# Kernel tuning notes

Hardware: AMD Instinct MI355X
Metric: run time of the kernel (lower is better)

Reference implementation:

```python
import jax, jax.numpy as jnp
import numpy as np

B, S, C, L = 8, 256, 4, 256
E, H, NL, NS = 256, 8, 2, 8
DH = E // H
EPS = 1e-5


def _conv1d(x, w, b):
    # x: [B, Cin, L], w: [Cout, Cin, K] -> [B, Cout, L] (SAME padding, stride 1)
    y = jax.lax.conv_general_dilated(x, w, (1,), 'SAME', dimension_numbers=('NCH', 'OIH', 'NCH'))
    return y + b[None, :, None]


def _local_cnn(xs, w1, b1, w2, b2):
    # xs: [B, 4, L] for one segment; per-segment weights
    h = jax.nn.relu(_conv1d(xs, w1, b1))
    h = jax.nn.relu(_conv1d(h, w2, b2))
    return jnp.max(h, axis=-1)  # AdaptiveMaxPool1d(1) + squeeze -> [B, E]


def _layernorm(x, g, b):
    m = jnp.mean(x, axis=-1, keepdims=True)
    v = jnp.mean((x - m) ** 2, axis=-1, keepdims=True)
    return (x - m) / jnp.sqrt(v + EPS) * g + b


def setup_inputs() -> dict:
    key = jax.random.key(0)
    ks = jax.random.split(key, 24)
    n = lambda k, shp, s: jax.random.normal(k, shp, jnp.float32) * s
    return {
        'x': jax.random.normal(ks[0], (B, S, C, L), jnp.float32),
        'conv1_w': n(ks[1], (S, 128, 4, 3), 0.1), 'conv1_b': jnp.zeros((S, 128), jnp.float32),
        'conv2_w': n(ks[2], (S, E, 128, 3), 0.05), 'conv2_b': jnp.zeros((S, E), jnp.float32),
        'ln1_g': jnp.ones((NL, E), jnp.float32), 'ln1_b': jnp.zeros((NL, E), jnp.float32),
        'wq': n(ks[3], (NL, E, E), 0.02), 'bq': jnp.zeros((NL, E), jnp.float32),
        'wk': n(ks[4], (NL, E, E), 0.02), 'bk': jnp.zeros((NL, E), jnp.float32),
        'wv': n(ks[5], (NL, E, E), 0.02), 'bv': jnp.zeros((NL, E), jnp.float32),
        'wo': n(ks[6], (NL, E, E), 0.02), 'bo': jnp.zeros((NL, E), jnp.float32),
        'bias_w': n(ks[7], (NL, 4, H), 0.1), 'bias_b': jnp.zeros((NL, H), jnp.float32),
        'ln2_g': jnp.ones((NL, E), jnp.float32), 'ln2_b': jnp.zeros((NL, E), jnp.float32),
        'ffn_w1': n(ks[8], (NL, E, 2 * E), 0.02), 'ffn_b1': jnp.zeros((NL, 2 * E), jnp.float32),
        'ffn_w2': n(ks[9], (NL, 2 * E, E), 0.02), 'ffn_b2': jnp.zeros((NL, E), jnp.float32),
        'fc_w': n(ks[10], (NS * E, 2), 0.02), 'fc_b': jnp.zeros((2,), jnp.float32),
    }


def _forward(x, conv1_w, conv1_b, conv2_w, conv2_b, ln1_g, ln1_b,
             wq, bq, wk, bk, wv, bv, wo, bo, bias_w, bias_b,
             ln2_g, ln2_b, ffn_w1, ffn_b1, ffn_w2, ffn_b2, fc_w, fc_b):
    # Per-segment CNNs (vmap over segment axis with per-segment weights) -> [B, S, E]
    cnn = jax.vmap(_local_cnn, in_axes=(1, 0, 0, 0, 0), out_axes=1)(x, conv1_w, conv1_b, conv2_w, conv2_b)
    feat = _layernorm(cnn, jnp.ones((E,), cnn.dtype), jnp.zeros((E,), cnn.dtype))  # F.layer_norm, no affine

    # bias matrices: cdist (p=2), global-max normalized; positional distance; inverses
    sq = jnp.sum(feat * feat, axis=-1)  # [B, S]
    d2 = sq[:, :, None] + sq[:, None, :] - 2.0 * jnp.einsum('bie,bje->bij', feat, feat)
    dist = jnp.sqrt(jnp.maximum(d2, 0.0))
    dist = dist / (jnp.max(dist) + 1e-6)
    idx = jnp.arange(S, dtype=feat.dtype)
    rdist = jnp.abs(idx[:, None] - idx[None, :]) / (S - 1)
    rdist = jnp.broadcast_to(rdist[None], (feat.shape[0], S, S))
    attn_bias = jnp.stack([dist, rdist, 1.0 - rdist, 1.0 - dist], axis=-1)  # [B,S,S,4]

    h = feat
    scale = 1.0 / jnp.sqrt(jnp.asarray(DH, h.dtype))
    for l in range(NL):
        hn = _layernorm(h, ln1_g[l], ln1_b[l])
        q = (hn @ wq[l] + bq[l]).reshape(-1, S, H, DH)
        k = (hn @ wk[l] + bk[l]).reshape(-1, S, H, DH)
        v = (hn @ wv[l] + bv[l]).reshape(-1, S, H, DH)
        scores = jnp.einsum('bihd,bjhd->bhij', q, k) * scale
        scores = scores + jnp.einsum('bijc,ch->bhij', attn_bias, bias_w[l]) + bias_b[l][None, :, None, None]
        a = jax.nn.softmax(scores, axis=-1)
        o = jnp.einsum('bhij,bjhd->bihd', a, v).reshape(-1, S, E) @ wo[l] + bo[l]
        h = h + o
        hn2 = _layernorm(h, ln2_g[l], ln2_b[l])
        f = jax.nn.relu(hn2 @ ffn_w1[l] + ffn_b1[l]) @ ffn_w2[l] + ffn_b2[l]
        h = h + f

    # split into NS chunks along segments, max-pool each, concat (S % NS == 0)
    pooled = jnp.max(h.reshape(-1, NS, S // NS, E), axis=2).reshape(-1, NS * E)
    return pooled @ fc_w + fc_b  # [B, num_classes]


def reference(x, conv1_w, conv1_b, conv2_w, conv2_b, ln1_g, ln1_b,
              wq, bq, wk, bk, wv, bv, wo, bo, bias_w, bias_b,
              ln2_g, ln2_b, ffn_w1, ffn_b1, ffn_w2, ffn_b2, fc_w, fc_b):
    return _forward(x, conv1_w, conv1_b, conv2_w, conv2_b, ln1_g, ln1_b,
                    wq, bq, wk, bk, wv, bv, wo, bo, bias_w, bias_b,
                    ln2_g, ln2_b, ffn_w1, ffn_b1, ffn_w2, ffn_b2, fc_w, fc_b)
```

## Files before the change

kernel.cpp:

```cpp
#include <hip/hip_runtime.h>
#include <hip/hip_bf16.h>


typedef float floatx4 __attribute__((ext_vector_type(4)));
typedef short bf16x8 __attribute__((ext_vector_type(8)));

__device__ __forceinline__ float wave_sum(float v) {
    v += __shfl_xor(v, 32); v += __shfl_xor(v, 16); v += __shfl_xor(v, 8);
    v += __shfl_xor(v, 4);  v += __shfl_xor(v, 2);  v += __shfl_xor(v, 1);
    return v;
}
__device__ __forceinline__ float wave_max(float v) {
    v = fmaxf(v, __shfl_xor(v, 32)); v = fmaxf(v, __shfl_xor(v, 16));
    v = fmaxf(v, __shfl_xor(v, 8));  v = fmaxf(v, __shfl_xor(v, 4));
    v = fmaxf(v, __shfl_xor(v, 2));  v = fmaxf(v, __shfl_xor(v, 1));
    return v;
}
__device__ __forceinline__ unsigned short f2bf(float v) {
    unsigned b = __float_as_uint(v);
    unsigned r = (b + 0x7fffu + ((b >> 16) & 1u)) >> 16;
    return (unsigned short)r;
}

typedef const __attribute__((address_space(1))) unsigned int* gas_u32p;
typedef __attribute__((address_space(3))) unsigned int* las_u32p;

__device__ __forceinline__ void stage_chunk(const unsigned short* gbase,
                                            unsigned short* lbase,
                                            int wv, int lane)
{
    const char* g = (const char*)gbase + (wv << 11) + (lane << 4);
    char* l = (char*)lbase + (wv << 11);
    __builtin_amdgcn_global_load_lds((gas_u32p)(const void*)g,
                                     (las_u32p)(void*)l, 16, 0, 0);
    __builtin_amdgcn_global_load_lds((gas_u32p)(const void*)(g + 1024),
                                     (las_u32p)(void*)(l + 1024), 16, 0, 0);
}

__global__ void init_kernel(unsigned* dmax, unsigned* cnnmax) {
    const size_t i = (size_t)blockIdx.x * 256 + threadIdx.x;
    cnnmax[i] = 0u;
    if (i == 0) *dmax = 0u;
}

__global__ __launch_bounds__(256) void prep_w2_kernel(
    const float* __restrict__ w2, unsigned short* __restrict__ w2b)
{
    const int s = blockIdx.x;
    const int part = blockIdx.y;
    const float* src = w2 + (size_t)s * 98304;
    unsigned short* dst = w2b + (size_t)s * 98304;
    for (int o = part * 24576 + threadIdx.x; o < (part + 1) * 24576; o += 256) {
        const int c  = o >> 13;
        const int w  = o & 8191;
        const int co = w >> 5;
        const int up = (w >> 3) & 3;
        const int t  = w & 7;
        const int u  = (up ^ co ^ (co >> 2)) & 3;
        const int kk = c * 32 + u * 8 + t;
        const int ci = kk & 127, tap = kk >> 7;
        dst[o] = f2bf(src[(size_t)co * 384 + ci * 3 + tap]);
    }
}

__global__ __launch_bounds__(512, 4) void conv2_fused_kernel(
    const unsigned short* __restrict__ w2b,
    const float* __restrict__ x,
    const float* __restrict__ w1,
    const float* __restrict__ b1,
    const float* __restrict__ b2,
    unsigned* __restrict__ cnnmax)
{
    __shared__ float xs[4][258];
    __shared__ float w1s[1536];
    __shared__ unsigned short Hs[130 * 136];
    __shared__ unsigned short Ab[2][8192];

    const int tid = threadIdx.x;
    const int lane = tid & 63;
    const int wv = __builtin_amdgcn_readfirstlane((int)(tid >> 6));
    const int wm = wv & 3, wn = wv >> 2;
    const int bid = blockIdx.x;
    const int xcd = bid & 7;
    const int pos = bid >> 3;
    const int s   = xcd * 32 + (pos >> 4);
    const int nt  = pos & 15;
    const int b = nt >> 1;
    const int l0 = (nt & 1) * 128;
    const int lr = lane & 15;
    const int quad = lane >> 4;
    const int qk = quad * 8;

    const float* xp = x + ((size_t)(b * 256 + s)) * 1024;
    for (int i = tid; i < 1024; i += 512) {
        const int ci = i >> 8, l = i & 255;
        xs[ci][l + 1] = xp[i];
    }
    if (tid < 4) { xs[tid][0] = 0.f; xs[tid][257] = 0.f; }
    const float* w1p = w1 + (size_t)s * 1536;
    for (int i = tid; i < 1536; i += 512) w1s[i] = w1p[i];
    const int co1 = tid & 127;
    const float bb1 = b1[s * 128 + co1];
    __syncthreads();

    const unsigned short* wchunks = w2b + (size_t)s * 98304;
    stage_chunk(wchunks, &Ab[0][0], wv, lane);

    {
        const int g = tid >> 7;
        float wreg[12];
#pragma unroll
        for (int k = 0; k < 12; k++) wreg[k] = w1s[co1 * 12 + k];
        for (int pr = g; pr < 130; pr += 4) {
            const int l = l0 - 1 + pr;
            float a = 0.f;
            if ((unsigned)l < 256u) {
                a = bb1;
#pragma unroll
                for (int ci = 0; ci < 4; ci++)
#pragma unroll
                    for (int k = 0; k < 3; k++) a = fmaf(wreg[ci * 3 + k], xs[ci][l + k], a);
                a = fmaxf(a, 0.f);
            }
            Hs[pr * 136 + co1] = f2bf(a);
        }
    }

    floatx4 acc[4][4];
#pragma unroll
    for (int r = 0; r < 4; r++)
#pragma unroll
        for (int c = 0; c < 4; c++) acc[r][c] = (floatx4){0.f, 0.f, 0.f, 0.f};

    const int nb = wn * 64;
    const int aoff = wm * 2048 + lr * 32 + (((quad ^ lr ^ (lr >> 2)) & 3) * 8);
    const int hbase = (nb + lr) * 136 + qk;

    asm volatile("s_waitcnt vmcnt(0) lgkmcnt(0)" ::: "memory");
    __builtin_amdgcn_s_barrier();
    __builtin_amdgcn_sched_barrier(0);

#pragma unroll
    for (int ks = 0; ks < 12; ks++) {
        if (ks) {
            asm volatile("s_waitcnt vmcnt(0)" ::: "memory");
            __builtin_amdgcn_s_barrier();
            __builtin_amdgcn_sched_barrier(0);
        }
        if (ks < 11)
            stage_chunk(wchunks + (size_t)(ks + 1) * 8192, &Ab[(ks + 1) & 1][0], wv, lane);
        const int tap_ = ks >> 2, ci0_ = (ks & 3) * 32;
        const unsigned short* ap = &Ab[ks & 1][aoff];
        const unsigned short* hp = &Hs[hbase + tap_ * 136 + ci0_];
        bf16x8 a[4], bb[4];
#pragma unroll
        for (int r = 0; r < 4; r++) a[r] = *(const bf16x8*)(ap + r * 512);
#pragma unroll
        for (int c = 0; c < 4; c++) bb[c] = *(const bf16x8*)(hp + c * 2176);
#pragma unroll
        for (int r = 0; r < 4; r++)
#pragma unroll
            for (int c = 0; c < 4; c++)
                acc[r][c] = __builtin_amdgcn_mfma_f32_16x16x32_bf16(
                    a[r], bb[c], acc[r][c], 0, 0, 0);
    }

    const float* b2s = b2 + s * 256;
    unsigned* cmrow = cnnmax + ((size_t)(b * 256 + s)) * 256;
#pragma unroll
    for (int r = 0; r < 4; r++) {
#pragma unroll
        for (int e = 0; e < 4; e++) {
            const int co = wm * 64 + r * 16 + quad * 4 + e;
            const float bias = b2s[co];
            float mv = 0.f;
#pragma unroll
            for (int c = 0; c < 4; c++) mv = fmaxf(mv, acc[r][c][e] + bias);
            mv = fmaxf(mv, __shfl_xor(mv, 1));
            mv = fmaxf(mv, __shfl_xor(mv, 2));
            mv = fmaxf(mv, __shfl_xor(mv, 4));
            mv = fmaxf(mv, __shfl_xor(mv, 8));
            if (lr == 0) atomicMax(&cmrow[co], __float_as_uint(mv));
        }
    }
}

__global__ __launch_bounds__(256) void ln0_kernel(
    const unsigned* __restrict__ cm, float* __restrict__ out, float* __restrict__ sqv)
{
    const int tid = threadIdx.x, lane = tid & 63, wid = tid >> 6;
    const int row = blockIdx.x * 4 + wid;
    const unsigned* xr = cm + (size_t)row * 256;
    float v[4];
#pragma unroll
    for (int i = 0; i < 4; i++) v[i] = __uint_as_float(xr[lane + 64 * i]);
    float sm = wave_sum(v[0] + v[1] + v[2] + v[3]);
    const float mean = sm * (1.f / 256.f);
    float qv = 0.f;
#pragma unroll
    for (int i = 0; i < 4; i++) { const float d = v[i] - mean; qv = fmaf(d, d, qv); }
    qv = wave_sum(qv);
    const float inv = rsqrtf(qv * (1.f / 256.f) + 1e-5f);
    float* orow = out + (size_t)row * 256;
#pragma unroll
    for (int i = 0; i < 4; i++) orow[lane + 64 * i] = (v[i] - mean) * inv;
    if (lane == 0) sqv[row] = qv * inv * inv;
}

__global__ __launch_bounds__(256) void dist_kernel(
    const float* __restrict__ feat, const float* __restrict__ sq,
    float* __restrict__ dist, unsigned* __restrict__ dmax)
{
    __shared__ float Fi[32][260];
    __shared__ float Fj[16][260];
    __shared__ float redm[4];
    const int tid = threadIdx.x;
    const int bid = blockIdx.x;
    const int b = bid >> 7, it = (bid >> 4) & 7, jt = bid & 15;
    const float* fb = feat + (size_t)b * 65536;
    for (int idx = tid; idx < 32 * 256; idx += 256) {
        const int r = idx >> 8, e = idx & 255;
        Fi[r][e] = fb[(it * 32 + r) * 256 + e];
    }
    for (int idx = tid; idx < 16 * 256; idx += 256) {
        const int r = idx >> 8, e = idx & 255;
        Fj[r][e] = fb[(jt * 16 + r) * 256 + e];
    }
    __syncthreads();
    const int ii = tid >> 3, j0 = (tid & 7) * 2;
    float acc[2] = {0.f, 0.f};
    for (int e = 0; e < 256; e += 4) {
        const float4 a = *(const float4*)&Fi[ii][e];
#pragma unroll
        for (int u = 0; u < 2; u++) {
            const float4 bv = *(const float4*)&Fj[j0 + u][e];
            acc[u] += a.x * bv.x + a.y * bv.y + a.z * bv.z + a.w * bv.w;
        }
    }
    const float sqi = sq[b * 256 + it * 32 + ii];
    float mymax = 0.f;
#pragma unroll
    for (int u = 0; u < 2; u++) {
        const float d2 = sqi + sq[b * 256 + jt * 16 + j0 + u] - 2.f * acc[u];
        const float d = sqrtf(fmaxf(d2, 0.f));
        dist[((size_t)b * 256 + it * 32 + ii) * 256 + jt * 16 + j0 + u] = d;
        mymax = fmaxf(mymax, d);
    }
    mymax = wave_max(mymax);
    if ((tid & 63) == 0) redm[tid >> 6] = mymax;
    __syncthreads();
    if (tid == 0) {
        const float m = fmaxf(fmaxf(redm[0], redm[1]), fmaxf(redm[2], redm[3]));
        atomicMax(dmax, __float_as_uint(m));
    }
}

__global__ __launch_bounds__(256) void ln_bf_kernel(
    const float* __restrict__ x, const float* __restrict__ g, const float* __restrict__ bta,
    unsigned short* __restrict__ out)
{
    const int tid = threadIdx.x, lane = tid & 63, wid = tid >> 6;
    const int row = blockIdx.x * 4 + wid;
    const float* xr = x + (size_t)row * 256;
    float v[4];
#pragma unroll
    for (int i = 0; i < 4; i++) v[i] = xr[lane + 64 * i];
    float sm = wave_sum(v[0] + v[1] + v[2] + v[3]);
    const float mean = sm * (1.f / 256.f);
    float q = 0.f;
#pragma unroll
    for (int i = 0; i < 4; i++) { const float d = v[i] - mean; q = fmaf(d, d, q); }
    q = wave_sum(q);
    const float inv = rsqrtf(q * (1.f / 256.f) + 1e-5f);
    unsigned short* orow = out + (size_t)row * 256;
#pragma unroll
    for (int i = 0; i < 4; i++) {
        const int e = lane + 64 * i;
        orow[e] = f2bf((v[i] - mean) * inv * g[e] + bta[e]);
    }
}

__global__ __launch_bounds__(256) void prep_wt_kernel(
    const float* __restrict__ wq, const float* __restrict__ wk, const float* __restrict__ wv,
    const float* __restrict__ wo, const float* __restrict__ f1, const float* __restrict__ f2,
    unsigned short* __restrict__ wtb)
{
    __shared__ float t[32][33];
    const int z = blockIdx.z;
    const int l = z / 6, id = z % 6;
    const float* src; int K_, N_; size_t doff;
    switch (id) {
        case 0:  src = wq + (size_t)l * 65536;  K_ = 256; N_ = 256; doff = 0;      break;
        case 1:  src = wk + (size_t)l * 65536;  K_ = 256; N_ = 256; doff = 65536;  break;
        case 2:  src = wv + (size_t)l * 65536;  K_ = 256; N_ = 256; doff = 131072; break;
        case 3:  src = wo + (size_t)l * 65536;  K_ = 256; N_ = 256; doff = 196608; break;
        case 4:  src = f1 + (size_t)l * 131072; K_ = 256; N_ = 512; doff = 262144; break;
        default: src = f2 + (size_t)l * 131072; K_ = 512; N_ = 256; doff = 393216; break;
    }
    const int k0 = blockIdx.x * 32, n0 = blockIdx.y * 32;
    if (k0 >= K_ || n0 >= N_) return;
    unsigned short* dst = wtb + (size_t)l * 524288 + doff;
    const int c = threadIdx.x & 31, rq = threadIdx.x >> 5;
#pragma unroll
    for (int i = 0; i < 4; i++) {
        const int r = rq + i * 8;
        t[r][c] = src[(size_t)(k0 + r) * N_ + n0 + c];
    }
    __syncthreads();
#pragma unroll
    for (int i = 0; i < 4; i++) {
        const int r = rq + i * 8;
        dst[(size_t)(n0 + r) * K_ + k0 + c] = f2bf(t[c][r]);
    }
}

__global__ __launch_bounds__(128) void gemm_mfma_kernel(
    const unsigned short* __restrict__ A, const unsigned short* __restrict__ Wt,
    const float* __restrict__ b0, const float* __restrict__ b1, const float* __restrict__ b2,
    const float* __restrict__ R, float* __restrict__ outf,
    unsigned short* __restrict__ o0, unsigned short* __restrict__ o1, unsigned short* __restrict__ o2,
    int K, int mode)
{
    const int tid = threadIdx.x;
    const int lane = tid & 63, lr = lane & 15, quad = lane >> 4;
    const int wv = __builtin_amdgcn_readfirstlane((int)(tid >> 6));
    const int m0 = blockIdx.x * 128 + wv * 64;
    const int n0 = blockIdx.y * 32;

    floatx4 acc[4][2];
#pragma unroll
    for (int r = 0; r < 4; r++)
#pragma unroll
        for (int c = 0; c < 2; c++) acc[r][c] = (floatx4){0.f, 0.f, 0.f, 0.f};

    const unsigned short* Ap = A + (size_t)(m0 + lr) * K + quad * 8;
    const unsigned short* Bp = Wt + (size_t)(n0 + lr) * K + quad * 8;
    const int nks = K >> 5;
#pragma unroll 4
    for (int ks = 0; ks < nks; ks++) {
        const int ko = ks * 32;
        bf16x8 a[4], b[2];
#pragma unroll
        for (int r = 0; r < 4; r++) a[r] = *(const bf16x8*)(Ap + (size_t)r * 16 * K + ko);
#pragma unroll
        for (int c = 0; c < 2; c++) b[c] = *(const bf16x8*)(Bp + (size_t)c * 16 * K + ko);
#pragma unroll
        for (int r = 0; r < 4; r++)
#pragma unroll
            for (int c = 0; c < 2; c++)
                acc[r][c] = __builtin_amdgcn_mfma_f32_16x16x32_bf16(a[r], b[c], acc[r][c], 0, 0, 0);
    }

    if (mode == 0) {
        const int which = n0 >> 8, nn0 = n0 & 255;
        if (which < 2) {
            unsigned short* op = which ? o1 : o0;
            const float* bp = which ? b1 : b0;
#pragma unroll
            for (int r = 0; r < 4; r++)
#pragma unroll
                for (int c = 0; c < 2; c++)
#pragma unroll
                    for (int e = 0; e < 4; e++) {
                        const int m = m0 + r * 16 + quad * 4 + e;
                        const int n = nn0 + c * 16 + lr;
                        op[(size_t)m * 256 + n] = f2bf(acc[r][c][e] + bp[n]);
                    }
        } else {
#pragma unroll
            for (int r = 0; r < 4; r++)
#pragma unroll
                for (int c = 0; c < 2; c++)
#pragma unroll
                    for (int e = 0; e < 4; e++) {
                        const int m = m0 + r * 16 + quad * 4 + e;
                        const int nn = nn0 + c * 16 + lr;
                        const int bb_ = m >> 8, j = m & 255, hh = nn >> 5, d = nn & 31;
                        o2[(size_t)((bb_ * 8 + hh) * 32 + d) * 256 + j] = f2bf(acc[r][c][e] + b2[nn]);
                    }
        }
    } else if (mode == 1) {
#pragma unroll
        for (int r = 0; r < 4; r++)
#pragma unroll
            for (int c = 0; c < 2; c++)
#pragma unroll
                for (int e = 0; e < 4; e++) {
                    const int m = m0 + r * 16 + quad * 4 + e;
                    const int n = n0 + c * 16 + lr;
                    outf[(size_t)m * 256 + n] = acc[r][c][e] + b0[n] + R[(size_t)m * 256 + n];
                }
    } else {
#pragma unroll
        for (int r = 0; r < 4; r++)
#pragma unroll
            for (int c = 0; c < 2; c++)
#pragma unroll
                for (int e = 0; e < 4; e++) {
                    const int m = m0 + r * 16 + quad * 4 + e;
                    const int n = n0 + c * 16 + lr;
                    o0[(size_t)m * 512 + n] = f2bf(fmaxf(acc[r][c][e] + b0[n], 0.f));
                }
    }
}

__global__ __launch_bounds__(256) void attn_mfma_kernel(
    const unsigned short* __restrict__ q_bf, const unsigned short* __restrict__ k_bf,
    const unsigned short* __restrict__ vt_bf,
    const float* __restrict__ dist, const unsigned* __restrict__ dmax,
    const float* __restrict__ bw, const float* __restrict__ bb,
    unsigned short* __restrict__ ao_bf)
{
    __shared__ unsigned short Ps[4][16][264];
    const int tid = threadIdx.x;
    const int lane = tid & 63, lr = lane & 15, quad = lane >> 4;
    const int wv = __builtin_amdgcn_readfirstlane((int)(tid >> 6));
    const int ic = blockIdx.x, hh = blockIdx.y, b = blockIdx.z;
    const int i0 = ic * 64 + wv * 16;

    const float dinv = 1.f / (__uint_as_float(*dmax) + 1e-6f);
    const float w0 = bw[0 * 8 + hh], w1 = bw[1 * 8 + hh], w2 = bw[2 * 8 + hh], w3 = bw[3 * 8 + hh];
    const float bbh = bb[hh];
    const float scale = 0.17677669529663687f;

    const bf16x8 aq = *(const bf16x8*)(q_bf + (size_t)(b * 256 + i0 + lr) * 256 + hh * 32 + quad * 8);
    floatx4 sc[16];
#pragma unroll
    for (int c = 0; c < 16; c++) {
        const bf16x8 bk = *(const bf16x8*)(k_bf + (size_t)(b * 256 + c * 16 + lr) * 256 + hh * 32 + quad * 8);
        sc[c] = __builtin_amdgcn_mfma_f32_16x16x32_bf16(aq, bk, (floatx4){0.f, 0.f, 0.f, 0.f}, 0, 0, 0);
    }

#pragma unroll
    for (int e = 0; e < 4; e++) {
        const int i = i0 + quad * 4 + e;
        const float* drow = dist + ((size_t)(b * 256 + i)) * 256;
        float bs[16];
        float mx = -1e30f;
#pragma unroll
        for (int c = 0; c < 16; c++) {
            const int j = c * 16 + lr;
            const float dn = drow[j] * dinv;
            const float rd = fabsf((float)(i - j)) * (1.f / 255.f);
            bs[c] = sc[c][e] * scale + w0 * dn + w1 * rd + w2 * (1.f - rd) + w3 * (1.f - dn) + bbh;
            mx = fmaxf(mx, bs[c]);
        }
        mx = fmaxf(mx, __shfl_xor(mx, 1)); mx = fmaxf(mx, __shfl_xor(mx, 2));
        mx = fmaxf(mx, __shfl_xor(mx, 4)); mx = fmaxf(mx, __shfl_xor(mx, 8));
        float sm = 0.f;
#pragma unroll
        for (int c = 0; c < 16; c++) { bs[c] = __expf(bs[c] - mx); sm += bs[c]; }
        sm += __shfl_xor(sm, 1); sm += __shfl_xor(sm, 2);
        sm += __shfl_xor(sm, 4); sm += __shfl_xor(sm, 8);
        const float rs = 1.f / sm;
#pragma unroll
        for (int c = 0; c < 16; c++)
            Ps[wv][quad * 4 + e][c * 16 + lr] = f2bf(bs[c] * rs);
    }
    __syncthreads();

    floatx4 oc[2];
    oc[0] = (floatx4){0.f, 0.f, 0.f, 0.f};
    oc[1] = (floatx4){0.f, 0.f, 0.f, 0.f};
    const unsigned short* vtb = vt_bf + (size_t)(b * 8 + hh) * 8192;
#pragma unroll
    for (int ks = 0; ks < 8; ks++) {
        const bf16x8 ap = *(const bf16x8*)(&Ps[wv][lr][ks * 32 + quad * 8]);
#pragma unroll
        for (int c2 = 0; c2 < 2; c2++) {
            const bf16x8 bvv = *(const bf16x8*)(vtb + (size_t)(c2 * 16 + lr) * 256 + ks * 32 + quad * 8);
            oc[c2] = __builtin_amdgcn_mfma_f32_16x16x32_bf16(ap, bvv, oc[c2], 0, 0, 0);
        }
    }
#pragma unroll
    for (int c2 = 0; c2 < 2; c2++)
#pragma unroll
        for (int e = 0; e < 4; e++)
            ao_bf[(size_t)(b * 256 + i0 + quad * 4 + e) * 256 + hh * 32 + c2 * 16 + lr] = f2bf(oc[c2][e]);
}

__global__ __launch_bounds__(256) void pool_fc_kernel(
    const float* __restrict__ h, const float* __restrict__ fcw,
    const float* __restrict__ fcb, float* __restrict__ out)
{
    __shared__ float red[8];
    const int b = blockIdx.x, tid = threadIdx.x, lane = tid & 63, wid = tid >> 6;
    float a0 = 0.f, a1 = 0.f;
    for (int ns = 0; ns < 8; ns++) {
        const float* hp = h + ((size_t)(b * 256 + ns * 32)) * 256 + tid;
        float m = hp[0];
#pragma unroll
        for (int r = 1; r < 32; r++) m = fmaxf(m, hp[(size_t)r * 256]);
        a0 = fmaf(m, fcw[(ns * 256 + tid) * 2 + 0], a0);
        a1 = fmaf(m, fcw[(ns * 256 + tid) * 2 + 1], a1);
    }
    a0 = wave_sum(a0);
    a1 = wave_sum(a1);
    if (lane == 0) { red[wid] = a0; red[4 + wid] = a1; }
    __syncthreads();
    if (tid == 0) out[b * 2 + 0] = red[0] + red[1] + red[2] + red[3] + fcb[0];
    if (tid == 1) out[b * 2 + 1] = red[4] + red[5] + red[6] + red[7] + fcb[1];
}

extern "C" void kernel_launch(void* const* d_in, const int* in_sizes, int n_in,
                              void* d_out, int out_size, void* d_ws, size_t ws_size,
                              hipStream_t stream)
{
    (void)in_sizes; (void)n_in; (void)out_size; (void)ws_size;
    const float* x       = (const float*)d_in[0];
    const float* conv1_w = (const float*)d_in[1];
    const float* conv1_b = (const float*)d_in[2];
    const float* conv2_w = (const float*)d_in[3];
    const float* conv2_b = (const float*)d_in[4];
    const float* ln1_g   = (const float*)d_in[5];
    const float* ln1_b   = (const float*)d_in[6];
    const float* wq = (const float*)d_in[7];  const float* bq = (const float*)d_in[8];
    const float* wk = (const float*)d_in[9];  const float* bk = (const float*)d_in[10];
    const float* wvp = (const float*)d_in[11]; const float* bv = (const float*)d_in[12];
    const float* wo = (const float*)d_in[13]; const float* bo = (const float*)d_in[14];
    const float* bias_w = (const float*)d_in[15];
    const float* bias_b = (const float*)d_in[16];
    const float* ln2_g  = (const float*)d_in[17];
    const float* ln2_b  = (const float*)d_in[18];
    const float* ffn_w1 = (const float*)d_in[19]; const float* ffn_b1 = (const float*)d_in[20];
    const float* ffn_w2 = (const float*)d_in[21]; const float* ffn_b2 = (const float*)d_in[22];
    const float* fc_w   = (const float*)d_in[23]; const float* fc_b = (const float*)d_in[24];
    float* out = (float*)d_out;

    float* ws = (float*)d_ws;
    float* h    = ws;
    float* dist = h + 524288;
    float* sqv  = dist + 524288;
    unsigned* dmax = (unsigned*)(sqv + 2048);
    unsigned* cnnmax = (unsigned*)(sqv + 2048 + 16);
    unsigned short* hn_bf = (unsigned short*)(sqv + 2048 + 16 + 524288);
    unsigned short* q_bf  = hn_bf + 524288;
    unsigned short* k_bf  = q_bf + 524288;
    unsigned short* vt_bf = k_bf + 524288;
    unsigned short* ao_bf = vt_bf + 524288;
    unsigned short* fm_bf = ao_bf + 524288;
    unsigned short* wtb   = fm_bf + 1048576;
    unsigned short* w2b   = wtb + 1048576;

    init_kernel<<<2048, 256, 0, stream>>>(dmax, cnnmax);
    prep_wt_kernel<<<dim3(16, 16, 12), 256, 0, stream>>>(wq, wk, wvp, wo, ffn_w1, ffn_w2, wtb);
    prep_w2_kernel<<<dim3(256, 4), 256, 0, stream>>>(conv2_w, w2b);
    conv2_fused_kernel<<<4096, 512, 0, stream>>>(
        w2b, x, conv1_w, conv1_b, conv2_b, cnnmax);
    ln0_kernel<<<512, 256, 0, stream>>>(cnnmax, h, sqv);
    dist_kernel<<<1024, 256, 0, stream>>>(h, sqv, dist, dmax);

    for (int l = 0; l < 2; l++) {
        const unsigned short* wqkvT = wtb + (size_t)l * 524288;
        const unsigned short* woT   = wqkvT + 196608;
        const unsigned short* f1T   = wqkvT + 262144;
        const unsigned short* f2T   = wqkvT + 393216;

        ln_bf_kernel<<<512, 256, 0, stream>>>(h, ln1_g + l * 256, ln1_b + l * 256, hn_bf);
        gemm_mfma_kernel<<<dim3(16, 24), 128, 0, stream>>>(
            hn_bf, wqkvT, bq + l * 256, bk + l * 256, bv + l * 256,
            nullptr, nullptr, q_bf, k_bf, vt_bf, 256, 0);
        attn_mfma_kernel<<<dim3(4, 8, 8), 256, 0, stream>>>(
            q_bf, k_bf, vt_bf, dist, dmax, bias_w + l * 32, bias_b + l * 8, ao_bf);
        gemm_mfma_kernel<<<dim3(16, 8), 128, 0, stream>>>(
            ao_bf, woT, bo + l * 256, nullptr, nullptr,
            h, h, nullptr, nullptr, nullptr, 256, 1);
        ln_bf_kernel<<<512, 256, 0, stream>>>(h, ln2_g + l * 256, ln2_b + l * 256, hn_bf);
        gemm_mfma_kernel<<<dim3(16, 16), 128, 0, stream>>>(
            hn_bf, f1T, ffn_b1 + l * 512, nullptr, nullptr,
            nullptr, nullptr, fm_bf, nullptr, nullptr, 256, 2);
        gemm_mfma_kernel<<<dim3(16, 8), 128, 0, stream>>>(
            fm_bf, f2T, ffn_b2 + l * 256, nullptr, nullptr,
            h, h, nullptr, nullptr, nullptr, 512, 1);
    }
    pool_fc_kernel<<<8, 256, 0, stream>>>(h, fc_w, fc_b, out);
}
```

Measured before the change: 568.2 us.

## Merge prep kernels, add MFMA setprio, shrink GEMM tiles for more blocks

Folds the init, weight-transpose and conv2-weight prep kernels into one launch that dispatches on block index, removing two launches. Wraps the conv2 MFMA loop in s_setprio so waves issuing matrix ops get scheduling priority. Halves the GEMM M tile per wave (64 to 32 rows) and doubles the grid, so the small transformer GEMMs spread across more CUs at the cost of reloading the B operand more often.

```diff
diff --git a/kernel.cpp b/kernel.cpp
--- a/kernel.cpp
+++ b/kernel.cpp
@@ -37,29 +37,73 @@
                                      (las_u32p)(void*)(l + 1024), 16, 0, 0);
 }
 
-__global__ void init_kernel(unsigned* dmax, unsigned* cnnmax) {
-    const size_t i = (size_t)blockIdx.x * 256 + threadIdx.x;
-    cnnmax[i] = 0u;
-    if (i == 0) *dmax = 0u;
-}
-
-__global__ __launch_bounds__(256) void prep_w2_kernel(
+__global__ __launch_bounds__(256) void prep_all_kernel(
+    unsigned* __restrict__ dmax, unsigned* __restrict__ cnnmax,
+    const float* __restrict__ wq, const float* __restrict__ wk,
+    const float* __restrict__ wv, const float* __restrict__ wo,
+    const float* __restrict__ f1, const float* __restrict__ f2,
+    unsigned short* __restrict__ wtb,
     const float* __restrict__ w2, unsigned short* __restrict__ w2b)
 {
-    const int s = blockIdx.x;
-    const int part = blockIdx.y;
-    const float* src = w2 + (size_t)s * 98304;
-    unsigned short* dst = w2b + (size_t)s * 98304;
-    for (int o = part * 24576 + threadIdx.x; o < (part + 1) * 24576; o += 256) {
-        const int c  = o >> 13;
-        const int w  = o & 8191;
-        const int co = w >> 5;
-        const int up = (w >> 3) & 3;
-        const int t  = w & 7;
-        const int u  = (up ^ co ^ (co >> 2)) & 3;
-        const int kk = c * 32 + u * 8 + t;
-        const int ci = kk & 127, tap = kk >> 7;
-        dst[o] = f2bf(src[(size_t)co * 384 + ci * 3 + tap]);
+    __shared__ float t[32][33];
+    const int bid = blockIdx.x;
+    const int tid = threadIdx.x;
+
+    if (bid < 2048) {
+        const size_t i = (size_t)bid * 256 + tid;
+        cnnmax[i] = 0u;
+        if (i == 0) *dmax = 0u;
+        return;
+    }
+    if (bid < 5120) {
+        const int idx = bid - 2048;
+        const int z = idx >> 8;
+        const int by = (idx >> 4) & 15;
+        const int bx = idx & 15;
+        const int l = z / 6, id = z % 6;
+        const float* src; int K_, N_; size_t doff;
+        switch (id) {
+            case 0:  src = wq + (size_t)l * 65536;  K_ = 256; N_ = 256; doff = 0;      break;
+            case 1:  src = wk + (size_t)l * 65536;  K_ = 256; N_ = 256; doff = 65536;  break;
+            case 2:  src = wv + (size_t)l * 65536;  K_ = 256; N_ = 256; doff = 131072; break;
+            case 3:  src = wo + (size_t)l * 65536;  K_ = 256; N_ = 256; doff = 196608; break;
+            case 4:  src = f1 + (size_t)l * 131072; K_ = 256; N_ = 512; doff = 262144; break;
+            default: src = f2 + (size_t)l * 131072; K_ = 512; N_ = 256; doff = 393216; break;
+        }
+        const int k0 = bx * 32, n0 = by * 32;
+        if (k0 >= K_ || n0 >= N_) return;
+        unsigned short* dst = wtb + (size_t)l * 524288 + doff;
+        const int c = tid & 31, rq = tid >> 5;
+#pragma unroll
+        for (int i = 0; i < 4; i++) {
+            const int r = rq + i * 8;
+            t[r][c] = src[(size_t)(k0 + r) * N_ + n0 + c];
+        }
+        __syncthreads();
+#pragma unroll
+        for (int i = 0; i < 4; i++) {
+            const int r = rq + i * 8;
+            dst[(size_t)(n0 + r) * K_ + k0 + c] = f2bf(t[c][r]);
+        }
+        return;
+    }
+    {
+        const int idx = bid - 5120;
+        const int s = idx & 255;
+        const int part = idx >> 8;
+        const float* src = w2 + (size_t)s * 98304;
+        unsigned short* dst = w2b + (size_t)s * 98304;
+        for (int o = part * 24576 + tid; o < (part + 1) * 24576; o += 256) {
+            const int c  = o >> 13;
+            const int w  = o & 8191;
+            const int co = w >> 5;
+            const int up = (w >> 3) & 3;
+            const int tt = w & 7;
+            const int u  = (up ^ co ^ (co >> 2)) & 3;
+            const int kk = c * 32 + u * 8 + tt;
+            const int ci = kk & 127, tap = kk >> 7;
+            dst[o] = f2bf(src[(size_t)co * 384 + ci * 3 + tap]);
+        }
     }
 }
 
@@ -157,12 +201,14 @@
         for (int r = 0; r < 4; r++) a[r] = *(const bf16x8*)(ap + r * 512);
 #pragma unroll
         for (int c = 0; c < 4; c++) bb[c] = *(const bf16x8*)(hp + c * 2176);
+        __builtin_amdgcn_s_setprio(1);
 #pragma unroll
         for (int r = 0; r < 4; r++)
 #pragma unroll
             for (int c = 0; c < 4; c++)
                 acc[r][c] = __builtin_amdgcn_mfma_f32_16x16x32_bf16(
                     a[r], bb[c], acc[r][c], 0, 0, 0);
+        __builtin_amdgcn_s_setprio(0);
     }
 
     const float* b2s = b2 + s * 256;
@@ -280,40 +326,6 @@
     }
 }
 
-__global__ __launch_bounds__(256) void prep_wt_kernel(
-    const float* __restrict__ wq, const float* __restrict__ wk, const float* __restrict__ wv,
-    const float* __restrict__ wo, const float* __restrict__ f1, const float* __restrict__ f2,
-    unsigned short* __restrict__ wtb)
-{
-    __shared__ float t[32][33];
-    const int z = blockIdx.z;
-    const int l = z / 6, id = z % 6;
-    const float* src; int K_, N_; size_t doff;
-    switch (id) {
-        case 0:  src = wq + (size_t)l * 65536;  K_ = 256; N_ = 256; doff = 0;      break;
-        case 1:  src = wk + (size_t)l * 65536;  K_ = 256; N_ = 256; doff = 65536;  break;
-        case 2:  src = wv + (size_t)l * 65536;  K_ = 256; N_ = 256; doff = 131072; break;
-        case 3:  src = wo + (size_t)l * 65536;  K_ = 256; N_ = 256; doff = 196608; break;
-        case 4:  src = f1 + (size_t)l * 131072; K_ = 256; N_ = 512; doff = 262144; break;
-        default: src = f2 + (size_t)l * 131072; K_ = 512; N_ = 256; doff = 393216; break;
-    }
-    const int k0 = blockIdx.x * 32, n0 = blockIdx.y * 32;
-    if (k0 >= K_ || n0 >= N_) return;
-    unsigned short* dst = wtb + (size_t)l * 524288 + doff;
-    const int c = threadIdx.x & 31, rq = threadIdx.x >> 5;
-#pragma unroll
-    for (int i = 0; i < 4; i++) {
-        const int r = rq + i * 8;
-        t[r][c] = src[(size_t)(k0 + r) * N_ + n0 + c];
-    }
-    __syncthreads();
-#pragma unroll
-    for (int i = 0; i < 4; i++) {
-        const int r = rq + i * 8;
-        dst[(size_t)(n0 + r) * K_ + k0 + c] = f2bf(t[c][r]);
-    }
-}
-
 __global__ __launch_bounds__(128) void gemm_mfma_kernel(
     const unsigned short* __restrict__ A, const unsigned short* __restrict__ Wt,
     const float* __restrict__ b0, const float* __restrict__ b1, const float* __restrict__ b2,
@@ -324,12 +336,12 @@
     const int tid = threadIdx.x;
     const int lane = tid & 63, lr = lane & 15, quad = lane >> 4;
     const int wv = __builtin_amdgcn_readfirstlane((int)(tid >> 6));
-    const int m0 = blockIdx.x * 128 + wv * 64;
+    const int m0 = blockIdx.x * 64 + wv * 32;
     const int n0 = blockIdx.y * 32;
 
-    floatx4 acc[4][2];
-#pragma unroll
-    for (int r = 0; r < 4; r++)
+    floatx4 acc[2][2];
+#pragma unroll
+    for (int r = 0; r < 2; r++)
 #pragma unroll
         for (int c = 0; c < 2; c++) acc[r][c] = (floatx4){0.f, 0.f, 0.f, 0.f};
 
@@ -339,13 +351,13 @@
 #pragma unroll 4
     for (int ks = 0; ks < nks; ks++) {
         const int ko = ks * 32;
-        bf16x8 a[4], b[2];
-#pragma unroll
-        for (int r = 0; r < 4; r++) a[r] = *(const bf16x8*)(Ap + (size_t)r * 16 * K + ko);
+        bf16x8 a[2], b[2];
+#pragma unroll
+        for (int r = 0; r < 2; r++) a[r] = *(const bf16x8*)(Ap + (size_t)r * 16 * K + ko);
 #pragma unroll
         for (int c = 0; c < 2; c++) b[c] = *(const bf16x8*)(Bp + (size_t)c * 16 * K + ko);
 #pragma unroll
-        for (int r = 0; r < 4; r++)
+        for (int r = 0; r < 2; r++)
 #pragma unroll
             for (int c = 0; c < 2; c++)
                 acc[r][c] = __builtin_amdgcn_mfma_f32_16x16x32_bf16(a[r], b[c], acc[r][c], 0, 0, 0);
@@ -357,7 +369,7 @@
             unsigned short* op = which ? o1 : o0;
             const float* bp = which ? b1 : b0;
 #pragma unroll
-            for (int r = 0; r < 4; r++)
+            for (int r = 0; r < 2; r++)
 #pragma unroll
                 for (int c = 0; c < 2; c++)
 #pragma unroll
@@ -368,7 +380,7 @@
                     }
         } else {
 #pragma unroll
-            for (int r = 0; r < 4; r++)
+            for (int r = 0; r < 2; r++)
 #pragma unroll
                 for (int c = 0; c < 2; c++)
 #pragma unroll
@@ -381,7 +393,7 @@
         }
     } else if (mode == 1) {
 #pragma unroll
-        for (int r = 0; r < 4; r++)
+        for (int r = 0; r < 2; r++)
 #pragma unroll
             for (int c = 0; c < 2; c++)
 #pragma unroll
@@ -392,7 +404,7 @@
                 }
     } else {
 #pragma unroll
-        for (int r = 0; r < 4; r++)
+        for (int r = 0; r < 2; r++)
 #pragma unroll
             for (int c = 0; c < 2; c++)
 #pragma unroll
@@ -542,9 +554,8 @@
     unsigned short* wtb   = fm_bf + 1048576;
     unsigned short* w2b   = wtb + 1048576;
 
-    init_kernel<<<2048, 256, 0, stream>>>(dmax, cnnmax);
-    prep_wt_kernel<<<dim3(16, 16, 12), 256, 0, stream>>>(wq, wk, wvp, wo, ffn_w1, ffn_w2, wtb);
-    prep_w2_kernel<<<dim3(256, 4), 256, 0, stream>>>(conv2_w, w2b);
+    prep_all_kernel<<<6144, 256, 0, stream>>>(
+        dmax, cnnmax, wq, wk, wvp, wo, ffn_w1, ffn_w2, wtb, conv2_w, w2b);
     conv2_fused_kernel<<<4096, 512, 0, stream>>>(
         w2b, x, conv1_w, conv1_b, conv2_b, cnnmax);
     ln0_kernel<<<512, 256, 0, stream>>>(cnnmax, h, sqv);
@@ -557,19 +568,19 @@
         const unsigned short* f2T   = wqkvT + 393216;
 
         ln_bf_kernel<<<512, 256, 0, stream>>>(h, ln1_g + l * 256, ln1_b + l * 256, hn_bf);
-        gemm_mfma_kernel<<<dim3(16, 24), 128, 0, stream>>>(
+        gemm_mfma_kernel<<<dim3(32, 24), 128, 0, stream>>>(
             hn_bf, wqkvT, bq + l * 256, bk + l * 256, bv + l * 256,
             nullptr, nullptr, q_bf, k_bf, vt_bf, 256, 0);
         attn_mfma_kernel<<<dim3(4, 8, 8), 256, 0, stream>>>(
             q_bf, k_bf, vt_bf, dist, dmax, bias_w + l * 32, bias_b + l * 8, ao_bf);
-        gemm_mfma_kernel<<<dim3(16, 8), 128, 0, stream>>>(
+        gemm_mfma_kernel<<<dim3(32, 8), 128, 0, stream>>>(
             ao_bf, woT, bo + l * 256, nullptr, nullptr,
             h, h, nullptr, nullptr, nullptr, 256, 1);
         ln_bf_kernel<<<512, 256, 0, stream>>>(h, ln2_g + l * 256, ln2_b + l * 256, hn_bf);
-        gemm_mfma_kernel<<<dim3(16, 16), 128, 0, stream>>>(
+        gemm_mfma_kernel<<<dim3(32, 16), 128, 0, stream>>>(
             hn_bf, f1T, ffn_b1 + l * 512, nullptr, nullptr,
             nullptr, nullptr, fm_bf, nullptr, nullptr, 256, 2);
-        gemm_mfma_kernel<<<dim3(16, 8), 128, 0, stream>>>(
+        gemm_mfma_kernel<<<dim3(32, 8), 128, 0, stream>>>(
             fm_bf, f2T, ffn_b2 + l * 256, nullptr, nullptr,
             h, h, nullptr, nullptr, nullptr, 512, 1);
     }
```

Measured after the change: 574.2 us. About the same (+1.1%).
